# Kernel tuning notes

Hardware: AMD Instinct MI355X
Metric: run time of the kernel (lower is better)

The kernel has to match this reference:

```python
import jax, jax.numpy as jnp
import numpy as np

B, T, U, P = 1024, 256, 512, 32


def setup_inputs() -> dict:
    key = jax.random.key(0)
    ks = jax.random.split(key, 6)
    s = 0.05
    return {
        "prices": jax.random.normal(ks[0], (B, T), dtype=jnp.float32),
        "Wx": jax.random.normal(ks[1], (1, 4 * U), dtype=jnp.float32) * s,
        "Wh": jax.random.normal(ks[2], (U, 4 * U), dtype=jnp.float32) * s,
        "b": jnp.zeros((4 * U,), dtype=jnp.float32),
        "Wd": jax.random.normal(ks[3], (U, 64), dtype=jnp.float32) * s,
        "bd": jnp.zeros((64,), dtype=jnp.float32),
        "Wp": jax.random.normal(ks[4], (64, P), dtype=jnp.float32) * s,
        "bp": jnp.zeros((P,), dtype=jnp.float32),
    }


def reference(prices, Wx, Wh, b, Wd, bd, Wp, bp):
    batch = prices.shape[0]
    units = Wh.shape[0]

    def cell(carry, x_t):
        h, c = carry  # [B,U] each
        z = x_t @ Wx + h @ Wh + b  # [B,4U]
        i, f, g, o = jnp.split(z, 4, axis=-1)
        i = jax.nn.sigmoid(i)
        f = jax.nn.sigmoid(f)
        g = jnp.tanh(g)
        o = jax.nn.sigmoid(o)
        c = f * c + i * g
        h = o * jnp.tanh(c)
        return (h, c), None

    h0 = jnp.zeros((batch, units), dtype=prices.dtype)
    c0 = jnp.zeros((batch, units), dtype=prices.dtype)
    xs = prices.T[:, :, None]  # [T,B,1]
    (h, _), _ = jax.lax.scan(cell, (h0, c0), xs)
    x = jax.nn.relu(h @ Wd + bd)  # [B,64]
    return x @ Wp + bp  # [B,P]
```

## Files before the change

### kernel.cpp

```cpp
#include <hip/hip_runtime.h>

typedef _Float16 half8 __attribute__((ext_vector_type(8)));
typedef float    f32x4 __attribute__((ext_vector_type(4)));
typedef unsigned int u32;
typedef unsigned long long u64;

#define B_   1024
#define T_   256
#define U_   512

#define PER_G  8
#define ROWS_G 32
#define U_WG   64
#define HS_LD  516

static const size_t WHT_OFF = 0;
static const size_t H_OFF   = 2u*1024*1024;
static const size_t CTR_OFF = 4u*1024*1024;
static const size_t PT_OFF  = 4u*1024*1024 + 65536;

__global__ __launch_bounds__(512)
void prep_wht(const float* __restrict__ Wh, _Float16* __restrict__ WhT) {
  int j = blockIdx.x;
  int k = threadIdx.x;
  WhT[(size_t)j*U_ + k] = (_Float16)Wh[(size_t)k*(4*U_) + j];
}

__global__ __launch_bounds__(256)
void prep_pt(const float* __restrict__ prices, float* __restrict__ pricesT) {
  int t = blockIdx.x;
  for (int r = threadIdx.x; r < B_; r += 256)
    pricesT[(size_t)t*B_ + r] = prices[(size_t)r*T_ + t];
}

__device__ __forceinline__ float sigm(float x) { return 1.f/(1.f + __expf(-x)); }
__device__ __forceinline__ float tanhf_fast(float x) {
  float ax = fabsf(x);
  float e  = __expf(2.f*ax);
  float t  = 1.f - 2.f/(e + 1.f);
  return copysignf(t, x);
}

__device__ __forceinline__ u64 ld_agent_u64(const void* p) {
  return __hip_atomic_load((const u64*)p, __ATOMIC_RELAXED, __HIP_MEMORY_SCOPE_AGENT);
}
__device__ __forceinline__ void st_agent_u64(void* p, u64 v) {
  __hip_atomic_store((u64*)p, v, __ATOMIC_RELAXED, __HIP_MEMORY_SCOPE_AGENT);
}
__device__ __forceinline__ void st_agent_u32(void* p, u32 v) {
  __hip_atomic_store((u32*)p, v, __ATOMIC_RELAXED, __HIP_MEMORY_SCOPE_AGENT);
}
__device__ __forceinline__ u32 ld_agent_u32(const void* p) {
  return __hip_atomic_load((const u32*)p, __ATOMIC_RELAXED, __HIP_MEMORY_SCOPE_AGENT);
}

__device__ __forceinline__ u64 ld_stage_u64(const void* p) {
  u64 v;
  asm volatile("global_load_dwordx2 %0, %1, off sc0 sc1" : "=v"(v) : "v"(p));
  return v;
}
__device__ __forceinline__ void vm_drain() {
  asm volatile("s_waitcnt vmcnt(0)" ::: "memory");
  __builtin_amdgcn_sched_barrier(0);
}

__global__ __launch_bounds__(512, 1)
void lstm_persist(const float* __restrict__ pricesT,
                  const float* __restrict__ Wx,
                  const float* __restrict__ bias,
                  const float* __restrict__ Wd,
                  const float* __restrict__ bd,
                  const float* __restrict__ Wp,
                  const float* __restrict__ bp,
                  const _Float16* __restrict__ WhT,
                  _Float16* __restrict__ hbuf,
                  u32* __restrict__ ctr,
                  float* __restrict__ out)
{
  __shared__ __align__(16) _Float16 hs[ROWS_G][HS_LD];
  __shared__ __align__(16) float    gz[4][ROWS_G][66];
  __shared__ float ps[ROWS_G];

  const int tid = threadIdx.x;
  const int b   = blockIdx.x;
  const int gid = b >> 3;
  const int j   = b & 7;
  const int row0 = gid * ROWS_G;
  const int u0   = j * U_WG;

  const int wv8 = tid >> 6;
  const int g   = wv8 & 3;
  const int cph = wv8 >> 2;
  const int ln  = tid & 15;
  const int qd  = (tid >> 4) & 3;

  half8 bf[16][2];
  #pragma unroll
  for (int kk = 0; kk < 16; ++kk) {
    #pragma unroll
    for (int ct = 0; ct < 2; ++ct) {
      int gcol = g*U_ + u0 + cph*32 + ct*16 + ln;
      bf[kk][ct] = *(const half8*)&WhT[(size_t)gcol*U_ + kk*32 + qd*8];
    }
  }

  const int grow = tid & 31;
  const int gu4  = (tid >> 5) * 4;
  float wxv[4][4], bv[4][4];
  #pragma unroll
  for (int gg = 0; gg < 4; ++gg)
    #pragma unroll
    for (int jj = 0; jj < 4; ++jj) {
      int ug = u0 + gu4 + jj;
      wxv[gg][jj] = Wx[gg*U_ + ug];
      bv[gg][jj]  = bias[gg*U_ + ug];
    }

  float c[4];
  #pragma unroll
  for (int e = 0; e < 4; ++e) c[e] = 0.f;

  u32* const myfl = ctr + gid*PER_G;

  for (int t = 0; t < T_; ++t) {
    const _Float16* hcur = hbuf + (size_t)(t & 1)*(B_*U_) + (size_t)row0*U_;
    _Float16* hnxt = hbuf + (size_t)((t + 1) & 1)*(B_*U_);

    if (wv8 == 0) {
      if (tid < ROWS_G) ps[tid] = pricesT[(size_t)t*B_ + row0 + tid];
      const int lane = tid & 63;
      bool ok;
      do {
        u32 v = (lane < PER_G) ? ld_agent_u32(&myfl[lane]) : 0xFFFFFFFFu;
        ok = (v >= (u32)t);
        if (!__all(ok)) { __builtin_amdgcn_s_sleep(1); ok = false; }
        else ok = true;
      } while (!ok);
    }
    __syncthreads();

    {
      u64 vbuf[8];
      #pragma unroll
      for (int it = 0; it < 8; ++it) {
        int id = tid + it*512;
        int r  = id >> 7;
        int ch = id & 127;
        vbuf[it] = ld_stage_u64(&hcur[(size_t)r*U_ + ch*4]);
      }
      vm_drain();
      #pragma unroll
      for (int it = 0; it < 8; ++it) {
        int id = tid + it*512;
        int r  = id >> 7;
        int ch = id & 127;
        *(u64*)&hs[r][ch*4] = vbuf[it];
      }
    }
    __syncthreads();

    f32x4 acc[2][2];
    #pragma unroll
    for (int rt = 0; rt < 2; ++rt)
      #pragma unroll
      for (int ct = 0; ct < 2; ++ct)
        #pragma unroll
        for (int r = 0; r < 4; ++r)
          acc[rt][ct][r] = 0.f;

    #pragma unroll
    for (int kk = 0; kk < 16; ++kk) {
      #pragma unroll
      for (int rt = 0; rt < 2; ++rt) {
        half8 afr = *(const half8*)&hs[rt*16 + ln][kk*32 + qd*8];
        acc[rt][0] = __builtin_amdgcn_mfma_f32_16x16x32_f16(afr, bf[kk][0], acc[rt][0], 0, 0, 0);
        acc[rt][1] = __builtin_amdgcn_mfma_f32_16x16x32_f16(afr, bf[kk][1], acc[rt][1], 0, 0, 0);
      }
    }

    #pragma unroll
    for (int rt = 0; rt < 2; ++rt)
      #pragma unroll
      for (int ct = 0; ct < 2; ++ct)
        #pragma unroll
        for (int r = 0; r < 4; ++r)
          gz[g][rt*16 + qd*4 + r][cph*32 + ct*16 + ln] = acc[rt][ct][r];
    __syncthreads();

    {
      float px = ps[grow];
      unsigned short hb[4];
      #pragma unroll
      for (int jj = 0; jj < 4; ++jj) {
        float zi = gz[0][grow][gu4+jj] + px*wxv[0][jj] + bv[0][jj];
        float zf = gz[1][grow][gu4+jj] + px*wxv[1][jj] + bv[1][jj];
        float zg = gz[2][grow][gu4+jj] + px*wxv[2][jj] + bv[2][jj];
        float zo = gz[3][grow][gu4+jj] + px*wxv[3][jj] + bv[3][jj];
        float ig = sigm(zi), fg = sigm(zf), gg = tanhf_fast(zg), og = sigm(zo);
        float cn = fg*c[jj] + ig*gg;
        c[jj] = cn;
        _Float16 hh = (_Float16)(og*tanhf_fast(cn));
        hb[jj] = __builtin_bit_cast(unsigned short, hh);
      }
      u64 pk = (u64)hb[0] | ((u64)hb[1] << 16) | ((u64)hb[2] << 32) | ((u64)hb[3] << 48);
      st_agent_u64(&hnxt[(size_t)(row0 + grow)*U_ + u0 + gu4], pk);
    }

    __syncthreads();
    if (tid == 0) st_agent_u32(&myfl[j], (u32)(t + 1));
  }

  if (wv8 == 0) {
    const int lane = tid & 63;
    bool ok;
    do {
      u32 v = (lane < PER_G) ? ld_agent_u32(&myfl[lane]) : 0xFFFFFFFFu;
      ok = (v >= (u32)T_);
      if (!__all(ok)) { __builtin_amdgcn_s_sleep(1); ok = false; }
      else ok = true;
    } while (!ok);
  }
  __syncthreads();

  {
    const _Float16* hfin = hbuf;
    float*    xrow = (float*)&gz[0][0][0];
    _Float16* hrow = (_Float16*)((char*)&gz[0][0][0] + 1024);

    {
      int fl = tid*4;
      int r2 = fl >> 9;
      int of = fl & 511;
      u64 v = ld_agent_u64(&hfin[(size_t)(row0 + j*4 + r2)*U_ + of]);
      *(u64*)&hrow[r2*U_ + of] = v;
    }
    __syncthreads();
    if (tid < 256) {
      int rr = tid >> 6;
      int kk = tid & 63;
      float a = bd[kk];
      for (int k2 = 0; k2 < U_; ++k2)
        a += (float)hrow[rr*U_ + k2] * Wd[(size_t)k2*64 + kk];
      a = fmaxf(a, 0.f);
      xrow[rr*64 + kk] = a;
    }
    __syncthreads();
    if (tid < 256 && (tid & 63) < 32) {
      int rr = tid >> 6;
      int kk = tid & 63;
      int brow = row0 + j*4 + rr;
      float o2 = bp[kk];
      #pragma unroll
      for (int j2 = 0; j2 < 64; ++j2)
        o2 += xrow[rr*64 + j2] * Wp[j2*32 + kk];
      out[(size_t)brow*32 + kk] = o2;
    }
  }
}

extern "C" void kernel_launch(void* const* d_in, const int* in_sizes, int n_in,
                              void* d_out, int out_size, void* d_ws, size_t ws_size,
                              hipStream_t stream) {
  (void)in_sizes; (void)n_in; (void)out_size; (void)ws_size;
  const float* prices = (const float*)d_in[0];
  const float* Wx     = (const float*)d_in[1];
  const float* Wh     = (const float*)d_in[2];
  const float* bias   = (const float*)d_in[3];
  const float* Wd     = (const float*)d_in[4];
  const float* bd     = (const float*)d_in[5];
  const float* Wp     = (const float*)d_in[6];
  const float* bp     = (const float*)d_in[7];

  char* ws = (char*)d_ws;
  _Float16* WhT  = (_Float16*)(ws + WHT_OFF);
  _Float16* hbuf = (_Float16*)(ws + H_OFF);
  u32* ctr       = (u32*)(ws + CTR_OFF);
  float* pricesT = (float*)(ws + PT_OFF);

  hipMemsetAsync(hbuf, 0, (size_t)B_*U_*sizeof(_Float16), stream);
  hipMemsetAsync(ctr, 0, 32*PER_G*sizeof(u32), stream);

  prep_wht<<<dim3(4*U_), dim3(U_), 0, stream>>>(Wh, WhT);
  prep_pt<<<dim3(T_), dim3(256), 0, stream>>>(prices, pricesT);
  lstm_persist<<<dim3(256), dim3(512), 0, stream>>>(pricesT, Wx, bias, Wd, bd, Wp, bp,
                                                    WhT, hbuf, ctr, (float*)d_out);
}
```

Before: 1.436 ms.

## Use per-wave flags and split h staging to overlap MFMA with loads

Replaces the per-workgroup step flag with per-wave flags (64 per group), so every wave polls readiness itself and signals after draining its own stores. This removes the trailing __syncthreads and the single-wave poll. The h-tile staging loads are split in two halves: the first half is written to LDS and consumed by the first eight k-steps of MFMA while the second half is still in flight. Prices go into a double-buffered LDS slot to avoid a race between steps. The cost is more polling traffic on the flag array (every wave reads 64 flags) and an extra barrier per step.

```diff
diff --git a/kernel.cpp b/kernel.cpp
--- a/kernel.cpp
+++ b/kernel.cpp
@@ -58,6 +58,10 @@
   u64 v;
   asm volatile("global_load_dwordx2 %0, %1, off sc0 sc1" : "=v"(v) : "v"(p));
   return v;
+}
+__device__ __forceinline__ void vm_wait4() {
+  asm volatile("s_waitcnt vmcnt(4)" ::: "memory");
+  __builtin_amdgcn_sched_barrier(0);
 }
 __device__ __forceinline__ void vm_drain() {
   asm volatile("s_waitcnt vmcnt(0)" ::: "memory");
@@ -79,7 +83,7 @@
 {
   __shared__ __align__(16) _Float16 hs[ROWS_G][HS_LD];
   __shared__ __align__(16) float    gz[4][ROWS_G][66];
-  __shared__ float ps[ROWS_G];
+  __shared__ float ps[2][ROWS_G];
 
   const int tid = threadIdx.x;
   const int b   = blockIdx.x;
@@ -93,6 +97,7 @@
   const int cph = wv8 >> 2;
   const int ln  = tid & 15;
   const int qd  = (tid >> 4) & 3;
+  const int lane = tid & 63;
 
   half8 bf[16][2];
   #pragma unroll
@@ -120,43 +125,38 @@
   #pragma unroll
   for (int e = 0; e < 4; ++e) c[e] = 0.f;
 
-  u32* const myfl = ctr + gid*PER_G;
+  u32* const gfl = ctr + gid*64;
+  const int r   = tid >> 4;
+  const int chh = (tid & 15) * 4;
 
   for (int t = 0; t < T_; ++t) {
     const _Float16* hcur = hbuf + (size_t)(t & 1)*(B_*U_) + (size_t)row0*U_;
     _Float16* hnxt = hbuf + (size_t)((t + 1) & 1)*(B_*U_);
 
-    if (wv8 == 0) {
-      if (tid < ROWS_G) ps[tid] = pricesT[(size_t)t*B_ + row0 + tid];
-      const int lane = tid & 63;
+    float psv = 0.f;
+    if (wv8 == 0 && tid < ROWS_G)
+      psv = pricesT[(size_t)t*B_ + row0 + tid];
+
+    {
       bool ok;
       do {
-        u32 v = (lane < PER_G) ? ld_agent_u32(&myfl[lane]) : 0xFFFFFFFFu;
+        u32 v = ld_agent_u32(&gfl[lane]);
         ok = (v >= (u32)t);
         if (!__all(ok)) { __builtin_amdgcn_s_sleep(1); ok = false; }
         else ok = true;
       } while (!ok);
     }
-    __syncthreads();
-
-    {
-      u64 vbuf[8];
-      #pragma unroll
-      for (int it = 0; it < 8; ++it) {
-        int id = tid + it*512;
-        int r  = id >> 7;
-        int ch = id & 127;
-        vbuf[it] = ld_stage_u64(&hcur[(size_t)r*U_ + ch*4]);
-      }
-      vm_drain();
-      #pragma unroll
-      for (int it = 0; it < 8; ++it) {
-        int id = tid + it*512;
-        int r  = id >> 7;
-        int ch = id & 127;
-        *(u64*)&hs[r][ch*4] = vbuf[it];
-      }
-    }
+    if (wv8 == 0 && tid < ROWS_G) ps[t & 1][tid] = psv;
+
+    u64 vbuf[8];
+    #pragma unroll
+    for (int s = 0; s < 8; ++s)
+      vbuf[s] = ld_stage_u64(&hcur[(size_t)r*U_ + s*64 + chh]);
+
+    vm_wait4();
+    #pragma unroll
+    for (int s = 0; s < 4; ++s)
+      *(u64*)&hs[r][s*64 + chh] = vbuf[s];
     __syncthreads();
 
     f32x4 acc[2][2];
@@ -165,11 +165,11 @@
       #pragma unroll
       for (int ct = 0; ct < 2; ++ct)
         #pragma unroll
-        for (int r = 0; r < 4; ++r)
-          acc[rt][ct][r] = 0.f;
-
-    #pragma unroll
-    for (int kk = 0; kk < 16; ++kk) {
+        for (int q = 0; q < 4; ++q)
+          acc[rt][ct][q] = 0.f;
+
+    #pragma unroll
+    for (int kk = 0; kk < 8; ++kk) {
       #pragma unroll
       for (int rt = 0; rt < 2; ++rt) {
         half8 afr = *(const half8*)&hs[rt*16 + ln][kk*32 + qd*8];
@@ -178,17 +178,33 @@
       }
     }
 
+    vm_drain();
+    #pragma unroll
+    for (int s = 4; s < 8; ++s)
+      *(u64*)&hs[r][s*64 + chh] = vbuf[s];
+    __syncthreads();
+
+    #pragma unroll
+    for (int kk = 8; kk < 16; ++kk) {
+      #pragma unroll
+      for (int rt = 0; rt < 2; ++rt) {
+        half8 afr = *(const half8*)&hs[rt*16 + ln][kk*32 + qd*8];
+        acc[rt][0] = __builtin_amdgcn_mfma_f32_16x16x32_f16(afr, bf[kk][0], acc[rt][0], 0, 0, 0);
+        acc[rt][1] = __builtin_amdgcn_mfma_f32_16x16x32_f16(afr, bf[kk][1], acc[rt][1], 0, 0, 0);
+      }
+    }
+
     #pragma unroll
     for (int rt = 0; rt < 2; ++rt)
       #pragma unroll
       for (int ct = 0; ct < 2; ++ct)
         #pragma unroll
-        for (int r = 0; r < 4; ++r)
-          gz[g][rt*16 + qd*4 + r][cph*32 + ct*16 + ln] = acc[rt][ct][r];
+        for (int q = 0; q < 4; ++q)
+          gz[g][rt*16 + qd*4 + q][cph*32 + ct*16 + ln] = acc[rt][ct][q];
     __syncthreads();
 
     {
-      float px = ps[grow];
+      float px = ps[t & 1][grow];
       unsigned short hb[4];
       #pragma unroll
       for (int jj = 0; jj < 4; ++jj) {
@@ -206,15 +222,14 @@
       st_agent_u64(&hnxt[(size_t)(row0 + grow)*U_ + u0 + gu4], pk);
     }
 
-    __syncthreads();
-    if (tid == 0) st_agent_u32(&myfl[j], (u32)(t + 1));
+    vm_drain();
+    if (lane == 0) st_agent_u32(&gfl[j*8 + wv8], (u32)(t + 1));
   }
 
-  if (wv8 == 0) {
-    const int lane = tid & 63;
+  {
     bool ok;
     do {
-      u32 v = (lane < PER_G) ? ld_agent_u32(&myfl[lane]) : 0xFFFFFFFFu;
+      u32 v = ld_agent_u32(&gfl[lane]);
       ok = (v >= (u32)T_);
       if (!__all(ok)) { __builtin_amdgcn_s_sleep(1); ok = false; }
       else ok = true;
@@ -278,7 +293,7 @@
   float* pricesT = (float*)(ws + PT_OFF);
 
   hipMemsetAsync(hbuf, 0, (size_t)B_*U_*sizeof(_Float16), stream);
-  hipMemsetAsync(ctr, 0, 32*PER_G*sizeof(u32), stream);
+  hipMemsetAsync(ctr, 0, 32*PER_G*8*sizeof(u32), stream);
 
   prep_wht<<<dim3(4*U_), dim3(U_), 0, stream>>>(Wh, WhT);
   prep_pt<<<dim3(T_), dim3(256), 0, stream>>>(prices, pricesT);
```

After: 1.865 ms. 29.9% more time.
